# Optimization experiments

Measured on AMD Instinct MI355X. Metric: run time of the kernel, lower is better.

The kernel has to match this reference:

```python
import jax, jax.numpy as jnp
import numpy as np

N = 131072
L = 300  # lan_vec_len

def _boxes(k):
    k1, k2, k3, k4 = jax.random.split(k, 4)
    x1 = jax.random.uniform(k1, (N,)) * 500.0
    y1 = jax.random.uniform(k2, (N,)) * 500.0
    w = 1.0 + jax.random.uniform(k3, (N,)) * 200.0
    h = 1.0 + jax.random.uniform(k4, (N,)) * 200.0
    return x1, y1, x1 + w, y1 + h

def setup_inputs() -> dict:
    key = jax.random.key(0)
    ks = jax.random.split(key, 10)
    sbj_vec = jax.random.normal(ks[0], (N, L), jnp.float32)
    obj_vec = jax.random.normal(ks[1], (N, L), jnp.float32)
    sx1, sy1, sx2, sy2 = _boxes(ks[2])
    ox1, oy1, ox2, oy2 = _boxes(ks[3])
    label = jax.random.randint(ks[4], (N,), 0, 2).astype(jnp.float32)
    misc = jax.random.uniform(ks[5], (N,))
    # rlts columns: [0:4 misc, 4 label, 5:9 sbj box, 9 misc, 10:14 obj box, 14 misc]
    rlts = jnp.stack([misc, misc, misc, misc, label,
                      sx1, sy1, sx2, sy2, misc,
                      ox1, oy1, ox2, oy2, misc], axis=1)
    spa_w = jax.random.normal(ks[6], (8, 1), jnp.float32) * 0.1
    spa_b = jnp.zeros((1,), jnp.float32)
    lan_w1 = jax.random.normal(ks[7], (2 * L, L), jnp.float32) * 0.05
    lan_b1 = jnp.zeros((L,), jnp.float32)
    lan_w2 = jax.random.normal(ks[8], (L, 1), jnp.float32) * 0.05
    lan_b2 = jnp.zeros((1,), jnp.float32)
    return {"sbj_vec": sbj_vec, "obj_vec": obj_vec, "rlts": rlts,
            "spa_w": spa_w, "spa_b": spa_b,
            "lan_w1": lan_w1, "lan_b1": lan_b1,
            "lan_w2": lan_w2, "lan_b2": lan_b2}

def _ext_box_feat(rlts):
    sb = rlts[:, 5:9]
    ob = rlts[:, 10:14]
    sw = sb[:, 2] - sb[:, 0]
    sh = sb[:, 3] - sb[:, 1]
    ow = ob[:, 2] - ob[:, 0]
    oh = ob[:, 3] - ob[:, 1]
    sbj = jnp.stack([(sb[:, 0] - ob[:, 0]) / sw,
                     (sb[:, 1] - ob[:, 1]) / sh,
                     jnp.log(sw / ow), jnp.log(sh / oh)], axis=1)
    obj = jnp.stack([(ob[:, 0] - sb[:, 0]) / ow,
                     (ob[:, 1] - sb[:, 1]) / oh,
                     jnp.log(ow / sw), jnp.log(oh / sh)], axis=1)
    return sbj, obj

def reference(sbj_vec, obj_vec, rlts, spa_w, spa_b, lan_w1, lan_b1, lan_w2, lan_b2):
    sbj_box, obj_box = _ext_box_feat(rlts)
    lan_feat = jnp.concatenate([sbj_vec, obj_vec], axis=1)        # [N, 2L]
    box_feat = jnp.concatenate([sbj_box, obj_box], axis=1)        # [N, 8]
    # lan_stream: ReLU -> (Dropout: identity in eval) -> Linear -> ReLU -> Linear
    h = jax.nn.relu(lan_feat)
    h = jax.nn.relu(h @ lan_w1 + lan_b1)
    lan_scores = h @ lan_w2 + lan_b2                              # [N, 1]
    box_scores = box_feat @ spa_w + spa_b                         # [N, 1]
    scores = jax.nn.sigmoid(lan_scores + box_scores)              # [N, 1]
    ys = (rlts[:, 4] > 0).astype(scores.dtype)                    # [N]
    s = scores[:, 0]
    # binary cross entropy (mean), clamped like torch's BCE
    log_s = jnp.clip(jnp.log(jnp.clip(s, 1e-12, 1.0)), -100.0)
    log_1s = jnp.clip(jnp.log(jnp.clip(1.0 - s, 1e-12, 1.0)), -100.0)
    loss = -jnp.mean(ys * log_s + (1.0 - ys) * log_1s)
    # faithful replication of loss_test's (buggy) counting logic, vectorized
    neg = ys == 0
    pos = ~neg
    N_pos = jnp.sum(pos.astype(jnp.float32))
    N_neg = jnp.sum(neg.astype(jnp.float32))
    N_pos_right = jnp.sum((neg & (s >= 0.5)).astype(jnp.float32))
    N_neg_right = jnp.sum((pos & (s < 0.5)).astype(jnp.float32))
    recall_pos = N_pos_right / N_pos
    recall_neg = N_neg_right / N_neg
    recall_all = (N_pos_right + N_neg_right) / (N_pos + N_neg)
    return scores, loss, recall_pos, recall_neg, recall_all
```

## Files before the change

### kernel.cpp

```cpp
#include <hip/hip_runtime.h>

constexpr int NROWS  = 131072;
constexpr int LDIM   = 300;
constexpr int KDIM   = 600;
constexpr int NPAD   = 320;
constexpr int KGRP   = 76;
constexpr int MTILE  = 64;
constexpr int NBLKS  = NROWS / MTILE;
constexpr int KSTEPS = 19;
constexpr int WT_ELEMS = KGRP * NPAD * 8;
constexpr size_t PART_OFF = 393216;
constexpr int ASTRIDE = 40;

typedef __bf16 bf16x8 __attribute__((ext_vector_type(8)));
typedef float  f32x4  __attribute__((ext_vector_type(4)));

__device__ __forceinline__ unsigned short f2bf(float f) {
    unsigned u = __float_as_uint(f);
    u += 0x7fffu + ((u >> 16) & 1u);
    return (unsigned short)(u >> 16);
}

__global__ void prep_w1(const float* __restrict__ w1, unsigned short* __restrict__ wt) {
    int idx = blockIdx.x * 256 + threadIdx.x;
    if (idx >= WT_ELEMS) return;
    int j    = idx & 7;
    int rest = idx >> 3;
    int n    = rest % NPAD;
    int kg   = rest / NPAD;
    int k    = kg * 8 + j;
    float v = 0.f;
    if (k < KDIM && n < LDIM) v = w1[k * LDIM + n];
    wt[idx] = f2bf(v);
}

__launch_bounds__(256, 2)
__global__ void main_kernel(const float* __restrict__ sbj, const float* __restrict__ obj,
                            const float* __restrict__ rlts,
                            const float* __restrict__ spa_w, const float* __restrict__ spa_b,
                            const float* __restrict__ b1, const float* __restrict__ w2,
                            const float* __restrict__ b2,
                            const unsigned short* __restrict__ wt,
                            float* __restrict__ out_scores, float* __restrict__ part) {
    __shared__ __attribute__((aligned(16))) short A_lds[2][MTILE * ASTRIDE];
    __shared__ float lanpart[4][MTILE];
    __shared__ float redbuf[4][8];

    const int tid  = threadIdx.x;
    const int lane = tid & 63;
    const int wv   = tid >> 6;
    const int l4   = lane & 15;
    const int q4   = lane >> 4;
    const int nbase = wv * 80;

    const int  blk  = blockIdx.x;
    const long row0 = (long)blk * MTILE;

    const int a_quad = tid & 7;
    const int a_row  = tid >> 3;

    f32x4 acc[4][5];
    #pragma unroll
    for (int rt = 0; rt < 4; ++rt)
        #pragma unroll
        for (int ct = 0; ct < 5; ++ct)
            acc[rt][ct] = (f32x4)(0.f);

    float4 pre[3][2];
    bf16x8 bfr[2][5];

    const unsigned short* wbase = wt + ((size_t)q4 * NPAD + nbase + l4) * 8;

    auto load_A = [&](int kt, int slot) {
        const int k0 = kt * 32 + a_quad * 4;
        #pragma unroll
        for (int i = 0; i < 2; ++i) {
            const long grow = row0 + a_row + i * 32;
            if (k0 < LDIM)       pre[slot][i] = *(const float4*)(sbj + grow * LDIM + k0);
            else if (k0 < KDIM)  pre[slot][i] = *(const float4*)(obj + grow * LDIM + (k0 - LDIM));
            else                 pre[slot][i] = make_float4(0.f, 0.f, 0.f, 0.f);
        }
    };
    auto load_B = [&](int kt, int rb) {
        #pragma unroll
        for (int ct = 0; ct < 5; ++ct)
            bfr[rb][ct] = *(const bf16x8*)(wbase + (size_t)kt * 4 * NPAD * 8 + ct * 16 * 8);
    };
    auto store_A = [&](int slot, int buf) {
        #pragma unroll
        for (int i = 0; i < 2; ++i) {
            const int row = a_row + i * 32;
            unsigned h0 = f2bf(fmaxf(pre[slot][i].x, 0.f));
            unsigned h1 = f2bf(fmaxf(pre[slot][i].y, 0.f));
            unsigned h2 = f2bf(fmaxf(pre[slot][i].z, 0.f));
            unsigned h3 = f2bf(fmaxf(pre[slot][i].w, 0.f));
            uint2 pk = make_uint2(h0 | (h1 << 16), h2 | (h3 << 16));
            *(uint2*)&A_lds[buf][row * ASTRIDE + a_quad * 4] = pk;
        }
    };

    load_B(0, 0);
    load_A(0, 0);
    load_A(1, 1);
    load_A(2, 2);
    store_A(0, 0);
    asm volatile("s_waitcnt lgkmcnt(0)" ::: "memory");
    __builtin_amdgcn_s_barrier();

    #pragma unroll
    for (int kt = 0; kt < KSTEPS; ++kt) {
        const int buf = kt & 1;

        bf16x8 af[4];
        #pragma unroll
        for (int rt = 0; rt < 4; ++rt)
            af[rt] = *(const bf16x8*)&A_lds[buf][(rt * 16 + l4) * ASTRIDE + q4 * 8];

        if (kt + 1 < KSTEPS) load_B(kt + 1, (kt + 1) & 1);
        if (kt + 3 < KSTEPS) load_A(kt + 3, kt % 3);

        #pragma unroll
        for (int ct = 0; ct < 5; ++ct)
            #pragma unroll
            for (int rt = 0; rt < 4; ++rt)
                acc[rt][ct] = __builtin_amdgcn_mfma_f32_16x16x32_bf16(af[rt], bfr[buf][ct], acc[rt][ct], 0, 0, 0);

        if (kt + 1 < KSTEPS) {
            store_A((kt + 1) % 3, buf ^ 1);
            asm volatile("s_waitcnt lgkmcnt(0)" ::: "memory");
            __builtin_amdgcn_s_barrier();
        }
    }

    float part_r[4][4];
    #pragma unroll
    for (int rt = 0; rt < 4; ++rt)
        #pragma unroll
        for (int r = 0; r < 4; ++r) part_r[rt][r] = 0.f;

    #pragma unroll
    for (int ct = 0; ct < 5; ++ct) {
        const int n = nbase + ct * 16 + l4;
        if (n < LDIM) {
            const float b1n = b1[n];
            const float w2n = w2[n];
            #pragma unroll
            for (int rt = 0; rt < 4; ++rt)
                #pragma unroll
                for (int r = 0; r < 4; ++r) {
                    float h = fmaxf(acc[rt][ct][r] + b1n, 0.f);
                    part_r[rt][r] = fmaf(h, w2n, part_r[rt][r]);
                }
        }
    }
    #pragma unroll
    for (int off = 1; off < 16; off <<= 1)
        #pragma unroll
        for (int rt = 0; rt < 4; ++rt)
            #pragma unroll
            for (int r = 0; r < 4; ++r)
                part_r[rt][r] += __shfl_xor(part_r[rt][r], off, 64);

    if (l4 == 0) {
        #pragma unroll
        for (int rt = 0; rt < 4; ++rt)
            #pragma unroll
            for (int r = 0; r < 4; ++r)
                lanpart[wv][rt * 16 + q4 * 4 + r] = part_r[rt][r];
    }
    __syncthreads();

    float s_loss = 0.f, s_cp = 0.f, s_cn = 0.f, s_pr = 0.f, s_nr = 0.f;
    if (tid < MTILE) {
        const long g   = row0 + tid;
        const float lan = lanpart[0][tid] + lanpart[1][tid] + lanpart[2][tid] + lanpart[3][tid] + b2[0];
        const float* rr = rlts + g * 15;
        const float label = rr[4];
        const float sx1 = rr[5],  sy1 = rr[6],  sx2 = rr[7],  sy2 = rr[8];
        const float ox1 = rr[10], oy1 = rr[11], ox2 = rr[12], oy2 = rr[13];
        const float sw = sx2 - sx1, sh = sy2 - sy1, ow = ox2 - ox1, oh = oy2 - oy1;
        float bs = spa_w[0] * ((sx1 - ox1) / sw)
                 + spa_w[1] * ((sy1 - oy1) / sh)
                 + spa_w[2] * logf(sw / ow)
                 + spa_w[3] * logf(sh / oh)
                 + spa_w[4] * ((ox1 - sx1) / ow)
                 + spa_w[5] * ((oy1 - sy1) / oh)
                 + spa_w[6] * logf(ow / sw)
                 + spa_w[7] * logf(oh / sh)
                 + spa_b[0];
        const float z = lan + bs;
        const float s = 1.f / (1.f + expf(-z));
        out_scores[g] = s;
        const float ls = fmaxf(logf(fminf(fmaxf(s, 1e-12f), 1.f)), -100.f);
        const float l1 = fmaxf(logf(fminf(fmaxf(1.f - s, 1e-12f), 1.f)), -100.f);
        const bool ys = label > 0.f;
        s_loss = ys ? ls : l1;
        s_cp   = ys ? 1.f : 0.f;
        s_cn   = ys ? 0.f : 1.f;
        s_pr   = (!ys && s >= 0.5f) ? 1.f : 0.f;
        s_nr   = (ys && s < 0.5f)  ? 1.f : 0.f;
    }
    #pragma unroll
    for (int off = 1; off < 64; off <<= 1) {
        s_loss += __shfl_xor(s_loss, off, 64);
        s_cp   += __shfl_xor(s_cp, off, 64);
        s_cn   += __shfl_xor(s_cn, off, 64);
        s_pr   += __shfl_xor(s_pr, off, 64);
        s_nr   += __shfl_xor(s_nr, off, 64);
    }
    if (lane == 0) {
        redbuf[wv][0] = s_loss; redbuf[wv][1] = s_cp; redbuf[wv][2] = s_cn;
        redbuf[wv][3] = s_pr;   redbuf[wv][4] = s_nr;
    }
    __syncthreads();
    if (tid == 0) {
        float t0 = 0.f, t1 = 0.f, t2 = 0.f, t3 = 0.f, t4 = 0.f;
        for (int w = 0; w < 4; ++w) {
            t0 += redbuf[w][0]; t1 += redbuf[w][1]; t2 += redbuf[w][2];
            t3 += redbuf[w][3]; t4 += redbuf[w][4];
        }
        part[blk * 8 + 0] = t0; part[blk * 8 + 1] = t1; part[blk * 8 + 2] = t2;
        part[blk * 8 + 3] = t3; part[blk * 8 + 4] = t4;
    }
}

__global__ void final_reduce(const float* __restrict__ part, float* __restrict__ out) {
    __shared__ float red[4][8];
    const int tid = threadIdx.x;
    const int lane = tid & 63, wv = tid >> 6;
    float a0 = 0.f, a1 = 0.f, a2 = 0.f, a3 = 0.f, a4 = 0.f;
    for (int b = tid; b < NBLKS; b += 256) {
        a0 += part[b * 8 + 0]; a1 += part[b * 8 + 1]; a2 += part[b * 8 + 2];
        a3 += part[b * 8 + 3]; a4 += part[b * 8 + 4];
    }
    #pragma unroll
    for (int off = 1; off < 64; off <<= 1) {
        a0 += __shfl_xor(a0, off, 64); a1 += __shfl_xor(a1, off, 64);
        a2 += __shfl_xor(a2, off, 64); a3 += __shfl_xor(a3, off, 64);
        a4 += __shfl_xor(a4, off, 64);
    }
    if (lane == 0) { red[wv][0] = a0; red[wv][1] = a1; red[wv][2] = a2; red[wv][3] = a3; red[wv][4] = a4; }
    __syncthreads();
    if (tid == 0) {
        float t0 = 0.f, t1 = 0.f, t2 = 0.f, t3 = 0.f, t4 = 0.f;
        for (int w = 0; w < 4; ++w) {
            t0 += red[w][0]; t1 += red[w][1]; t2 += red[w][2]; t3 += red[w][3]; t4 += red[w][4];
        }
        out[NROWS + 0] = -t0 / (float)NROWS;
        out[NROWS + 1] = t3 / t1;
        out[NROWS + 2] = t4 / t2;
        out[NROWS + 3] = (t3 + t4) / (t1 + t2);
    }
}

extern "C" void kernel_launch(void* const* d_in, const int* in_sizes, int n_in,
                              void* d_out, int out_size, void* d_ws, size_t ws_size,
                              hipStream_t stream) {
    const float* sbj   = (const float*)d_in[0];
    const float* obj   = (const float*)d_in[1];
    const float* rlts  = (const float*)d_in[2];
    const float* spa_w = (const float*)d_in[3];
    const float* spa_b = (const float*)d_in[4];
    const float* w1    = (const float*)d_in[5];
    const float* b1    = (const float*)d_in[6];
    const float* w2    = (const float*)d_in[7];
    const float* b2    = (const float*)d_in[8];
    float* out = (float*)d_out;

    unsigned short* wt = (unsigned short*)d_ws;
    float* part = (float*)((char*)d_ws + PART_OFF);

    prep_w1<<<(WT_ELEMS + 255) / 256, 256, 0, stream>>>(w1, wt);
    main_kernel<<<NBLKS, 256, 0, stream>>>(sbj, obj, rlts, spa_w, spa_b, b1, w2, b2, wt, out, part);
    final_reduce<<<1, 256, 0, stream>>>(part, out);
}
```

Measured before the change: 376.0 us.

## Stage A tiles in chunks of four K-steps to cut barriers

Restructures the main GEMM loop so each LDS stage holds four K-steps of the activation tile instead of one. Global prefetch and the LDS store with barrier now happen once per chunk, so there are 5 barriers instead of 19. The cost is four times the LDS footprint for A (about 20KB per block) and more prefetch registers, which may limit occupancy at 2 blocks per CU and reduce how finely memory latency overlaps with compute.

```diff
diff --git a/kernel.cpp b/kernel.cpp
--- a/kernel.cpp
+++ b/kernel.cpp
@@ -8,9 +8,11 @@
 constexpr int MTILE  = 64;
 constexpr int NBLKS  = NROWS / MTILE;
 constexpr int KSTEPS = 19;
+constexpr int CHUNK  = 4;
 constexpr int WT_ELEMS = KGRP * NPAD * 8;
 constexpr size_t PART_OFF = 393216;
 constexpr int ASTRIDE = 40;
+constexpr int STEPSH  = MTILE * ASTRIDE;
 
 typedef __bf16 bf16x8 __attribute__((ext_vector_type(8)));
 typedef float  f32x4  __attribute__((ext_vector_type(4)));
@@ -42,7 +44,7 @@
                             const float* __restrict__ b2,
                             const unsigned short* __restrict__ wt,
                             float* __restrict__ out_scores, float* __restrict__ part) {
-    __shared__ __attribute__((aligned(16))) short A_lds[2][MTILE * ASTRIDE];
+    __shared__ __attribute__((aligned(16))) short A_lds[2][CHUNK * STEPSH];
     __shared__ float lanpart[4][MTILE];
     __shared__ float redbuf[4][8];
 
@@ -66,12 +68,12 @@
         for (int ct = 0; ct < 5; ++ct)
             acc[rt][ct] = (f32x4)(0.f);
 
-    float4 pre[3][2];
+    float4 pre[CHUNK][2];
     bf16x8 bfr[2][5];
 
     const unsigned short* wbase = wt + ((size_t)q4 * NPAD + nbase + l4) * 8;
 
-    auto load_A = [&](int kt, int slot) {
+    auto ldA = [&](int kt, int slot) {
         const int k0 = kt * 32 + a_quad * 4;
         #pragma unroll
         for (int i = 0; i < 2; ++i) {
@@ -81,12 +83,7 @@
             else                 pre[slot][i] = make_float4(0.f, 0.f, 0.f, 0.f);
         }
     };
-    auto load_B = [&](int kt, int rb) {
-        #pragma unroll
-        for (int ct = 0; ct < 5; ++ct)
-            bfr[rb][ct] = *(const bf16x8*)(wbase + (size_t)kt * 4 * NPAD * 8 + ct * 16 * 8);
-    };
-    auto store_A = [&](int slot, int buf) {
+    auto stA = [&](int slot, int buf, int s) {
         #pragma unroll
         for (int i = 0; i < 2; ++i) {
             const int row = a_row + i * 32;
@@ -95,38 +92,55 @@
             unsigned h2 = f2bf(fmaxf(pre[slot][i].z, 0.f));
             unsigned h3 = f2bf(fmaxf(pre[slot][i].w, 0.f));
             uint2 pk = make_uint2(h0 | (h1 << 16), h2 | (h3 << 16));
-            *(uint2*)&A_lds[buf][row * ASTRIDE + a_quad * 4] = pk;
+            *(uint2*)&A_lds[buf][s * STEPSH + row * ASTRIDE + a_quad * 4] = pk;
         }
     };
-
-    load_B(0, 0);
-    load_A(0, 0);
-    load_A(1, 1);
-    load_A(2, 2);
-    store_A(0, 0);
+    auto ldB = [&](int u, int rb) {
+        #pragma unroll
+        for (int ct = 0; ct < 5; ++ct)
+            bfr[rb][ct] = *(const bf16x8*)(wbase + (size_t)u * 4 * NPAD * 8 + ct * 16 * 8);
+    };
+
+    ldB(0, 0);
+    #pragma unroll
+    for (int s = 0; s < CHUNK; ++s) ldA(s, s);
+    #pragma unroll
+    for (int s = 0; s < CHUNK; ++s) stA(s, 0, s);
     asm volatile("s_waitcnt lgkmcnt(0)" ::: "memory");
     __builtin_amdgcn_s_barrier();
 
     #pragma unroll
-    for (int kt = 0; kt < KSTEPS; ++kt) {
-        const int buf = kt & 1;
-
-        bf16x8 af[4];
-        #pragma unroll
-        for (int rt = 0; rt < 4; ++rt)
-            af[rt] = *(const bf16x8*)&A_lds[buf][(rt * 16 + l4) * ASTRIDE + q4 * 8];
-
-        if (kt + 1 < KSTEPS) load_B(kt + 1, (kt + 1) & 1);
-        if (kt + 3 < KSTEPS) load_A(kt + 3, kt % 3);
-
-        #pragma unroll
-        for (int ct = 0; ct < 5; ++ct)
+    for (int c = 0; c < 5; ++c) {
+        const int buf = c & 1;
+        const int s0  = c * CHUNK;
+        const int ns  = (c == 4) ? 3 : 4;
+        const int nn  = (c == 3) ? 3 : 4;
+
+        if (c < 4) {
+            #pragma unroll
+            for (int s = 0; s < nn; ++s) ldA(s0 + CHUNK + s, s);
+        }
+
+        #pragma unroll
+        for (int s = 0; s < ns; ++s) {
+            const int u = s0 + s;
+            bf16x8 af[4];
             #pragma unroll
             for (int rt = 0; rt < 4; ++rt)
-                acc[rt][ct] = __builtin_amdgcn_mfma_f32_16x16x32_bf16(af[rt], bfr[buf][ct], acc[rt][ct], 0, 0, 0);
-
-        if (kt + 1 < KSTEPS) {
-            store_A((kt + 1) % 3, buf ^ 1);
+                af[rt] = *(const bf16x8*)&A_lds[buf][s * STEPSH + (rt * 16 + l4) * ASTRIDE + q4 * 8];
+
+            if (u + 1 < KSTEPS) ldB(u + 1, (u + 1) & 1);
+
+            #pragma unroll
+            for (int ct = 0; ct < 5; ++ct)
+                #pragma unroll
+                for (int rt = 0; rt < 4; ++rt)
+                    acc[rt][ct] = __builtin_amdgcn_mfma_f32_16x16x32_bf16(af[rt], bfr[u & 1][ct], acc[rt][ct], 0, 0, 0);
+        }
+
+        if (c < 4) {
+            #pragma unroll
+            for (int s = 0; s < nn; ++s) stA(s, buf ^ 1, s);
             asm volatile("s_waitcnt lgkmcnt(0)" ::: "memory");
             __builtin_amdgcn_s_barrier();
         }
```

New measurement: 372.8 us. Within noise of the previous version (-0.9%).
